# Kernel tuning notes

Hardware: AMD Instinct MI355X
Metric: run time of the kernel (lower is better)

Reference implementation:

```python
import jax, jax.numpy as jnp
import numpy as np

N_HEAD, F_IN, F_OUT = 4, 768, 64
BS, N = 4, 2048


def setup_inputs() -> dict:
    key = jax.random.key(0)
    k_h, k_w, k_src, k_dst = jax.random.split(key, 4)
    # xavier_uniform bounds
    lim_w = float(np.sqrt(6.0 / (F_IN + F_OUT)))
    lim_a = float(np.sqrt(6.0 / (F_OUT + 1)))
    return {
        "h": jax.random.normal(k_h, (BS, N, F_IN), dtype=jnp.float32),
        "w": jax.random.uniform(k_w, (N_HEAD, F_IN, F_OUT), jnp.float32, -lim_w, lim_w),
        "a_src": jax.random.uniform(k_src, (N_HEAD, F_OUT, 1), jnp.float32, -lim_a, lim_a),
        "a_dst": jax.random.uniform(k_dst, (N_HEAD, F_OUT, 1), jnp.float32, -lim_a, lim_a),
        "bias": jnp.zeros((F_OUT,), dtype=jnp.float32),
    }


def reference(h, w, a_src, a_dst, bias):
    # h: [b, n, f_in]; w: [h, f_in, f_out]
    h_prime = jnp.einsum("bnf,hfo->bhno", h, w)          # [b, h, n, f_out]
    t = jnp.tanh(h_prime)
    attn_src = jnp.einsum("bhno,ho->bhn", t, a_src[..., 0])  # [b, h, n]
    attn_dst = jnp.einsum("bhno,ho->bhn", t, a_dst[..., 0])  # [b, h, n]
    # broadcast add: attn[b,h,i,j] = src[b,h,i] + dst[b,h,j]
    attn = attn_src[..., :, None] + attn_dst[..., None, :]   # [b, h, n, n]
    attn = jnp.where(attn >= 0, attn, 0.2 * attn)            # leaky_relu(0.2)
    attn = jax.nn.softmax(attn, axis=-1)
    out = jnp.einsum("bhij,bhjo->bhio", attn, h_prime)       # [b, h, n, f_out]
    return out + bias
```

## Files before the change

kernel.cpp:

```cpp
#include <hip/hip_runtime.h>
#include <hip/hip_bf16.h>

#define NHEAD 4
#define FIN   768
#define FOUT  64
#define BSZ   4
#define NSEQ  2048
#define BH    (BSZ*NHEAD)
#define LOG2E 1.44269504088896f

typedef __attribute__((ext_vector_type(8)))  short bf16x8;
typedef __attribute__((ext_vector_type(16))) float f32x16;
typedef __attribute__((ext_vector_type(8)))  unsigned short u16x8;
typedef __attribute__((ext_vector_type(4)))  unsigned short u16x4;
typedef __attribute__((ext_vector_type(4)))  unsigned u32x4;

__device__ __forceinline__ unsigned short f2bf(float f){
  unsigned b = __float_as_uint(f);
  return (unsigned short)((b + 0x7fffu + ((b >> 16) & 1u)) >> 16);
}
__device__ __forceinline__ float fexp2(float x){
#if __has_builtin(__builtin_amdgcn_exp2f)
  return __builtin_amdgcn_exp2f(x);
#else
  return exp2f(x);
#endif
}
__device__ __forceinline__ unsigned pkbf(float lo, float hi){
#if __has_builtin(__builtin_amdgcn_cvt_pk_bf16_f32)
  typedef __attribute__((ext_vector_type(2))) __bf16 bf2;
  union { bf2 v; unsigned u; } cv;
  cv.v = __builtin_amdgcn_cvt_pk_bf16_f32(lo, hi);
  return cv.u;
#else
  return (unsigned)f2bf(lo) | ((unsigned)f2bf(hi) << 16);
#endif
}
__device__ __forceinline__ float fast_tanh(float v){
  const float e = fexp2(v * (2.0f*LOG2E));
#if __has_builtin(__builtin_amdgcn_rcpf)
  return 1.0f - 2.0f*__builtin_amdgcn_rcpf(e + 1.0f);
#else
  return 1.0f - 2.0f/(e + 1.0f);
#endif
}

__global__ __launch_bounds__(512, 4) void k_hprime(
    const float* __restrict__ h, const float* __restrict__ w,
    const float* __restrict__ a_src, const float* __restrict__ a_dst,
    unsigned short* __restrict__ hpz2, float* __restrict__ srcv,
    float* __restrict__ dstv)
{
  __shared__ __align__(16) char smem[65536];
  float* psumS = (float*)(smem + 16384);
  float* psumD = (float*)(smem + 16896);
  char*  Tt    = smem + 32768;

  const int tid  = threadIdx.x;
  const int bid  = blockIdx.x;
  const int bh1  = (bid & 7) | (((bid >> 3) & 1) << 3);
  const int head = bh1 & 3;
  const int jbase = (bid >> 4) << 6;
  const int i0a   = (bh1 >> 2)*NSEQ + jbase;
  const int wave = tid >> 6, lane = tid & 63;
  const int wm = wave & 1, wn = (wave >> 1) & 1, kw = wave >> 2;
  const int l32 = lane & 31, h32 = lane >> 5;

  f32x16 acc = {0,0,0,0,0,0,0,0,0,0,0,0,0,0,0,0};

  const int sr = tid >> 3, sc = tid & 7;
  const float* hA = h + (size_t)(i0a + sr)*FIN + sc*8;
  const int aslot = (sc ^ (sr & 7)) << 4;

  const int ob = tid & 63, cc = tid >> 6;
  const float* wsrc = w + (size_t)head*FIN*FOUT + ob;
  const int bslot0 = ((cc & 7) ^ (ob & 7)) << 4;

  float4 ra0 = *(const float4*)(hA);
  float4 ra1 = *(const float4*)(hA + 4);
  float4 ra2 = *(const float4*)(hA + 64);
  float4 ra3 = *(const float4*)(hA + 68);
  float rb[16];
  #pragma unroll
  for (int j = 0; j < 8; ++j){
    rb[j]     = wsrc[(size_t)(cc*8 + j)*FOUT];
    rb[8 + j] = wsrc[(size_t)(64 + cc*8 + j)*FOUT];
  }

  for (int it = 0; it < 6; ++it){
    char* Ab = smem +         (it & 1)*16384;
    char* Bb = smem + 32768 + (it & 1)*16384;
    u32x4 pk0, pk1;
    pk0[0] = pkbf(ra0.x, ra0.y); pk0[1] = pkbf(ra0.z, ra0.w);
    pk0[2] = pkbf(ra1.x, ra1.y); pk0[3] = pkbf(ra1.z, ra1.w);
    pk1[0] = pkbf(ra2.x, ra2.y); pk1[1] = pkbf(ra2.z, ra2.w);
    pk1[2] = pkbf(ra3.x, ra3.y); pk1[3] = pkbf(ra3.z, ra3.w);
    u32x4 qb0, qb1;
    qb0[0] = pkbf(rb[0],  rb[1]);  qb0[1] = pkbf(rb[2],  rb[3]);
    qb0[2] = pkbf(rb[4],  rb[5]);  qb0[3] = pkbf(rb[6],  rb[7]);
    qb1[0] = pkbf(rb[8],  rb[9]);  qb1[1] = pkbf(rb[10], rb[11]);
    qb1[2] = pkbf(rb[12], rb[13]); qb1[3] = pkbf(rb[14], rb[15]);
    if (it < 5){
      const float* an = hA + (it+1)*128;
      ra0 = *(const float4*)(an);      ra1 = *(const float4*)(an + 4);
      ra2 = *(const float4*)(an + 64); ra3 = *(const float4*)(an + 68);
      const float* wn_ = wsrc + (size_t)(it+1)*128*FOUT;
      #pragma unroll
      for (int j = 0; j < 8; ++j){
        rb[j]     = wn_[(size_t)(cc*8 + j)*FOUT];
        rb[8 + j] = wn_[(size_t)(64 + cc*8 + j)*FOUT];
      }
    }
    *(u32x4*)(Ab + sr*256 + aslot)        = pk0;
    *(u32x4*)(Ab + sr*256 + 128 + aslot)  = pk1;
    *(u32x4*)(Bb + ob*256 +       bslot0) = qb0;
    *(u32x4*)(Bb + ob*256 + 128 + bslot0) = qb1;
    asm volatile("s_waitcnt lgkmcnt(0)" ::: "memory");
    __builtin_amdgcn_s_barrier();
    __builtin_amdgcn_sched_barrier(0);
    #pragma unroll
    for (int s = 0; s < 4; ++s){
      const int slot = (((s*2 + h32) ^ (l32 & 7)) << 4);
      bf16x8 av = *(const bf16x8*)(Ab + (wm*32 + l32)*256 + kw*128 + slot);
      bf16x8 bv = *(const bf16x8*)(Bb + (wn*32 + l32)*256 + kw*128 + slot);
      acc = __builtin_amdgcn_mfma_f32_32x32x16_bf16(av, bv, acc, 0, 0, 0);
    }
  }

  if (kw == 1) *(f32x16*)(smem + (size_t)((wave & 3)*64 + lane)*64) = acc;
  __syncthreads();
  if (kw == 0){
    acc += *(const f32x16*)(smem + (size_t)((wave & 3)*64 + lane)*64);
    const float as = a_src[head*64 + wn*32 + l32];
    const float ad = a_dst[head*64 + wn*32 + l32];
    #pragma unroll
    for (int rb2 = 0; rb2 < 4; ++rb2){
      const int jb = wm*32 + rb2*8 + h32*4;
      u16x4 c4;
      #pragma unroll
      for (int q = 0; q < 4; ++q){
        const float v = acc[rb2*4 + q];
        c4[q] = f2bf(v);
        const float t = fast_tanh(v);
        float ps = t*as, pd = t*ad;
        ps += __shfl_xor(ps, 1);  ps += __shfl_xor(ps, 2);  ps += __shfl_xor(ps, 4);
        ps += __shfl_xor(ps, 8);  ps += __shfl_xor(ps, 16);
        pd += __shfl_xor(pd, 1);  pd += __shfl_xor(pd, 2);  pd += __shfl_xor(pd, 4);
        pd += __shfl_xor(pd, 8);  pd += __shfl_xor(pd, 16);
        if (l32 == 0){
          psumS[(jb + q)*2 + wn] = ps;
          psumD[(jb + q)*2 + wn] = pd;
        }
      }
      const int orow = wn*32 + l32;
      const int slot = ((jb >> 3) & 7) ^ (orow & 7);
      *(u16x4*)(Tt + orow*128 + slot*16 + (jb & 7)*2) = c4;
    }
  }
  __syncthreads();

  {
    const int o = tid & 63, c = tid >> 6;
    u16x8 val = *(const u16x8*)(Tt + o*128 + ((c ^ (o & 7)) << 4));
    *(u16x8*)((char*)hpz2 + ((size_t)(bh1*256 + (jbase >> 3) + c)*64 + o)*16) = val;
  }
  if (tid < 64){
    srcv[(size_t)bh1*NSEQ + jbase + tid] = (psumS[tid*2] + psumS[tid*2 + 1]) * LOG2E;
    dstv[(size_t)bh1*NSEQ + jbase + tid] = (psumD[tid*2] + psumD[tid*2 + 1]) * LOG2E;
  }
}

__global__ __launch_bounds__(512, 4) void k_attn(
    const unsigned short* __restrict__ hpz2, const float* __restrict__ srcv,
    const float* __restrict__ dstv, const float* __restrict__ bias,
    float* __restrict__ out)
{
  __shared__ __align__(16) char smem[33792];
  float* Lbuf = (float*)(smem + 32768);

  const int tid = threadIdx.x;
  const int bid = blockIdx.x;
  const int bh  = (bid & 7) | (((bid >> 3) & 1) << 3);
  const int i0  = (bid >> 4) << 6;
  const int wave = tid >> 6, lane = tid & 63;
  const int wm = wave & 1, jw = wave >> 1;
  const int l32 = lane & 31, h32 = lane >> 5;

  const float s2 = srcv[(size_t)bh*NSEQ + i0 + wm*32 + l32];
  const float u_ = s2;
  const float v_ = 0.2f*s2;

  const u16x8* gp = (const u16x8*)((const char*)hpz2 + (size_t)bh*256*64*16);
  const u16x8* tp = gp + ((jw*4 + h32)*64 + l32);
  const float* dS = dstv + (size_t)bh*NSEQ + (jw*4 + h32)*8;

  f32x16 accO0 = {0,0,0,0,0,0,0,0,0,0,0,0,0,0,0,0};
  f32x16 accO1 = {0,0,0,0,0,0,0,0,0,0,0,0,0,0,0,0};
  float lpart = 0.f;

  u16x8 c0 = tp[0], c1 = tp[32], c2 = tp[128], c3 = tp[160];
  float4 d0 = *(const float4*)(dS);
  float4 d1 = *(const float4*)(dS + 4);
  float4 d2 = *(const float4*)(dS + 16);
  float4 d3 = *(const float4*)(dS + 20);

  for (int w = 0; w < 16; ++w){
    u16x8 n0, n1, n2, n3;
    float4 g0, g1, g2, g3;
    if (w < 15){
      const u16x8* np = tp + 1024;
      n0 = np[0]; n1 = np[32]; n2 = np[128]; n3 = np[160];
      const float* dN = dS + 128;
      g0 = *(const float4*)(dN);
      g1 = *(const float4*)(dN + 4);
      g2 = *(const float4*)(dN + 16);
      g3 = *(const float4*)(dN + 20);
    }
    {
      float e0 = fexp2(fmaxf(u_ + d0.x, fmaf(0.2f, d0.x, v_)));
      float e1 = fexp2(fmaxf(u_ + d0.y, fmaf(0.2f, d0.y, v_)));
      float e2 = fexp2(fmaxf(u_ + d0.z, fmaf(0.2f, d0.z, v_)));
      float e3 = fexp2(fmaxf(u_ + d0.w, fmaf(0.2f, d0.w, v_)));
      float e4 = fexp2(fmaxf(u_ + d1.x, fmaf(0.2f, d1.x, v_)));
      float e5 = fexp2(fmaxf(u_ + d1.y, fmaf(0.2f, d1.y, v_)));
      float e6 = fexp2(fmaxf(u_ + d1.z, fmaf(0.2f, d1.z, v_)));
      float e7 = fexp2(fmaxf(u_ + d1.w, fmaf(0.2f, d1.w, v_)));
      lpart += ((e0+e1)+(e2+e3)) + ((e4+e5)+(e6+e7));
      u32x4 pk;
      pk[0] = pkbf(e0, e1); pk[1] = pkbf(e2, e3);
      pk[2] = pkbf(e4, e5); pk[3] = pkbf(e6, e7);
      const bf16x8 pA = __builtin_bit_cast(bf16x8, pk);
      accO0 = __builtin_amdgcn_mfma_f32_32x32x16_bf16(pA, c0, accO0, 0, 0, 0);
      accO1 = __builtin_amdgcn_mfma_f32_32x32x16_bf16(pA, c1, accO1, 0, 0, 0);
    }
    {
      float e0 = fexp2(fmaxf(u_ + d2.x, fmaf(0.2f, d2.x, v_)));
      float e1 = fexp2(fmaxf(u_ + d2.y, fmaf(0.2f, d2.y, v_)));
      float e2 = fexp2(fmaxf(u_ + d2.z, fmaf(0.2f, d2.z, v_)));
      float e3 = fexp2(fmaxf(u_ + d2.w, fmaf(0.2f, d2.w, v_)));
      float e4 = fexp2(fmaxf(u_ + d3.x, fmaf(0.2f, d3.x, v_)));
      float e5 = fexp2(fmaxf(u_ + d3.y, fmaf(0.2f, d3.y, v_)));
      float e6 = fexp2(fmaxf(u_ + d3.z, fmaf(0.2f, d3.z, v_)));
      float e7 = fexp2(fmaxf(u_ + d3.w, fmaf(0.2f, d3.w, v_)));
      lpart += ((e0+e1)+(e2+e3)) + ((e4+e5)+(e6+e7));
      u32x4 pk;
      pk[0] = pkbf(e0, e1); pk[1] = pkbf(e2, e3);
      pk[2] = pkbf(e4, e5); pk[3] = pkbf(e6, e7);
      const bf16x8 pA = __builtin_bit_cast(bf16x8, pk);
      accO0 = __builtin_amdgcn_mfma_f32_32x32x16_bf16(pA, c2, accO0, 0, 0, 0);
      accO1 = __builtin_amdgcn_mfma_f32_32x32x16_bf16(pA, c3, accO1, 0, 0, 0);
    }
    tp += 1024; dS += 128;
    c0 = n0; c1 = n1; c2 = n2; c3 = n3;
    d0 = g0; d1 = g1; d2 = g2; d3 = g3;
  }

  lpart += __shfl_xor(lpart, 32);
  if (lane < 32) Lbuf[(wm*4 + jw)*32 + l32] = lpart;

  const float4 bia = *(const float4*)(bias + (tid & 15)*4);
  #pragma unroll
  for (int ph = 0; ph < 2; ++ph){
    __syncthreads();
    if (wm == ph){
      float* ob = (float*)smem;
      #pragma unroll
      for (int reg = 0; reg < 16; ++reg){
        const int m = (reg & 3) + 8*(reg >> 2) + 4*h32;
        ob[(jw*32 + m)*64 +      l32] = accO0[reg];
        ob[(jw*32 + m)*64 + 32 + l32] = accO1[reg];
      }
    }
    __syncthreads();
    {
      const int i = tid >> 4, o4 = (tid & 15)*4;
      const float* ob = (const float*)smem;
      float4 v0 = *(const float4*)(ob + (0*32 + i)*64 + o4);
      float4 v1 = *(const float4*)(ob + (1*32 + i)*64 + o4);
      float4 v2 = *(const float4*)(ob + (2*32 + i)*64 + o4);
      float4 v3 = *(const float4*)(ob + (3*32 + i)*64 + o4);
      const float l = Lbuf[(ph*4+0)*32 + i] + Lbuf[(ph*4+1)*32 + i]
                    + Lbuf[(ph*4+2)*32 + i] + Lbuf[(ph*4+3)*32 + i];
      const float r = 1.f / l;
      float4 res;
      res.x = (v0.x + v1.x + v2.x + v3.x)*r + bia.x;
      res.y = (v0.y + v1.y + v2.y + v3.y)*r + bia.y;
      res.z = (v0.z + v1.z + v2.z + v3.z)*r + bia.z;
      res.w = (v0.w + v1.w + v2.w + v3.w)*r + bia.w;
      *(float4*)(out + ((size_t)bh*NSEQ + i0 + ph*32 + i)*64 + o4) = res;
    }
  }
}

extern "C" void kernel_launch(void* const* d_in, const int* in_sizes, int n_in,
                              void* d_out, int out_size, void* d_ws, size_t ws_size,
                              hipStream_t stream)
{
  const float* h     = (const float*)d_in[0];
  const float* w     = (const float*)d_in[1];
  const float* a_src = (const float*)d_in[2];
  const float* a_dst = (const float*)d_in[3];
  const float* bias  = (const float*)d_in[4];
  float* out = (float*)d_out;

  char* ws = (char*)d_ws;
  unsigned short* hpz2 = (unsigned short*)ws;
  float* srcv = (float*)(ws + (4u<<20));
  float* dstv = (float*)(ws + (4u<<20) + (128u<<10));

  k_hprime<<<512, 512, 0, stream>>>(h, w, a_src, a_dst, hpz2, srcv, dstv);
  k_attn<<<512, 512, 0, stream>>>(hpz2, srcv, dstv, bias, out);
}
```

Baseline: 116.6 us.

## Process two query-row tiles per attention block to reuse loaded value tiles

```diff
diff --git a/kernel.cpp b/kernel.cpp
--- a/kernel.cpp
+++ b/kernel.cpp
@@ -170,33 +170,37 @@
   }
 }
 
-__global__ __launch_bounds__(512, 4) void k_attn(
+__global__ __launch_bounds__(512, 2) void k_attn(
     const unsigned short* __restrict__ hpz2, const float* __restrict__ srcv,
     const float* __restrict__ dstv, const float* __restrict__ bias,
     float* __restrict__ out)
 {
-  __shared__ __align__(16) char smem[33792];
-  float* Lbuf = (float*)(smem + 32768);
+  __shared__ __align__(16) char smem[34816];
+  float* LbufA = (float*)(smem + 32768);
+  float* LbufB = (float*)(smem + 33792);
 
   const int tid = threadIdx.x;
   const int bid = blockIdx.x;
   const int bh  = (bid & 7) | (((bid >> 3) & 1) << 3);
-  const int i0  = (bid >> 4) << 6;
+  const int i0  = (bid >> 4) << 7;
   const int wave = tid >> 6, lane = tid & 63;
   const int wm = wave & 1, jw = wave >> 1;
   const int l32 = lane & 31, h32 = lane >> 5;
 
-  const float s2 = srcv[(size_t)bh*NSEQ + i0 + wm*32 + l32];
-  const float u_ = s2;
-  const float v_ = 0.2f*s2;
+  const float sA = srcv[(size_t)bh*NSEQ + i0      + wm*32 + l32];
+  const float sB = srcv[(size_t)bh*NSEQ + i0 + 64 + wm*32 + l32];
+  const float uA = sA, vA = 0.2f*sA;
+  const float uB = sB, vB = 0.2f*sB;
 
   const u16x8* gp = (const u16x8*)((const char*)hpz2 + (size_t)bh*256*64*16);
   const u16x8* tp = gp + ((jw*4 + h32)*64 + l32);
   const float* dS = dstv + (size_t)bh*NSEQ + (jw*4 + h32)*8;
 
-  f32x16 accO0 = {0,0,0,0,0,0,0,0,0,0,0,0,0,0,0,0};
-  f32x16 accO1 = {0,0,0,0,0,0,0,0,0,0,0,0,0,0,0,0};
-  float lpart = 0.f;
+  f32x16 accA0 = {0,0,0,0,0,0,0,0,0,0,0,0,0,0,0,0};
+  f32x16 accA1 = {0,0,0,0,0,0,0,0,0,0,0,0,0,0,0,0};
+  f32x16 accB0 = {0,0,0,0,0,0,0,0,0,0,0,0,0,0,0,0};
+  f32x16 accB1 = {0,0,0,0,0,0,0,0,0,0,0,0,0,0,0,0};
+  float lpA = 0.f, lpB = 0.f;
 
   u16x8 c0 = tp[0], c1 = tp[32], c2 = tp[128], c3 = tp[160];
   float4 d0 = *(const float4*)(dS);
@@ -217,46 +221,80 @@
       g3 = *(const float4*)(dN + 20);
     }
     {
-      float e0 = fexp2(fmaxf(u_ + d0.x, fmaf(0.2f, d0.x, v_)));
-      float e1 = fexp2(fmaxf(u_ + d0.y, fmaf(0.2f, d0.y, v_)));
-      float e2 = fexp2(fmaxf(u_ + d0.z, fmaf(0.2f, d0.z, v_)));
-      float e3 = fexp2(fmaxf(u_ + d0.w, fmaf(0.2f, d0.w, v_)));
-      float e4 = fexp2(fmaxf(u_ + d1.x, fmaf(0.2f, d1.x, v_)));
-      float e5 = fexp2(fmaxf(u_ + d1.y, fmaf(0.2f, d1.y, v_)));
-      float e6 = fexp2(fmaxf(u_ + d1.z, fmaf(0.2f, d1.z, v_)));
-      float e7 = fexp2(fmaxf(u_ + d1.w, fmaf(0.2f, d1.w, v_)));
-      lpart += ((e0+e1)+(e2+e3)) + ((e4+e5)+(e6+e7));
-      u32x4 pk;
-      pk[0] = pkbf(e0, e1); pk[1] = pkbf(e2, e3);
-      pk[2] = pkbf(e4, e5); pk[3] = pkbf(e6, e7);
-      const bf16x8 pA = __builtin_bit_cast(bf16x8, pk);
-      accO0 = __builtin_amdgcn_mfma_f32_32x32x16_bf16(pA, c0, accO0, 0, 0, 0);
-      accO1 = __builtin_amdgcn_mfma_f32_32x32x16_bf16(pA, c1, accO1, 0, 0, 0);
+      float eA0 = fexp2(fmaxf(uA + d0.x, fmaf(0.2f, d0.x, vA)));
+      float eA1 = fexp2(fmaxf(uA + d0.y, fmaf(0.2f, d0.y, vA)));
+      float eA2 = fexp2(fmaxf(uA + d0.z, fmaf(0.2f, d0.z, vA)));
+      float eA3 = fexp2(fmaxf(uA + d0.w, fmaf(0.2f, d0.w, vA)));
+      float eA4 = fexp2(fmaxf(uA + d1.x, fmaf(0.2f, d1.x, vA)));
+      float eA5 = fexp2(fmaxf(uA + d1.y, fmaf(0.2f, d1.y, vA)));
+      float eA6 = fexp2(fmaxf(uA + d1.z, fmaf(0.2f, d1.z, vA)));
+      float eA7 = fexp2(fmaxf(uA + d1.w, fmaf(0.2f, d1.w, vA)));
+      lpA += ((eA0+eA1)+(eA2+eA3)) + ((eA4+eA5)+(eA6+eA7));
+      u32x4 pa;
+      pa[0] = pkbf(eA0, eA1); pa[1] = pkbf(eA2, eA3);
+      pa[2] = pkbf(eA4, eA5); pa[3] = pkbf(eA6, eA7);
+      const bf16x8 pA_ = __builtin_bit_cast(bf16x8, pa);
+      float eB0 = fexp2(fmaxf(uB + d0.x, fmaf(0.2f, d0.x, vB)));
+      float eB1 = fexp2(fmaxf(uB + d0.y, fmaf(0.2f, d0.y, vB)));
+      float eB2 = fexp2(fmaxf(uB + d0.z, fmaf(0.2f, d0.z, vB)));
+      float eB3 = fexp2(fmaxf(uB + d0.w, fmaf(0.2f, d0.w, vB)));
+      float eB4 = fexp2(fmaxf(uB + d1.x, fmaf(0.2f, d1.x, vB)));
+      float eB5 = fexp2(fmaxf(uB + d1.y, fmaf(0.2f, d1.y, vB)));
+      float eB6 = fexp2(fmaxf(uB + d1.z, fmaf(0.2f, d1.z, vB)));
+      float eB7 = fexp2(fmaxf(uB + d1.w, fmaf(0.2f, d1.w, vB)));
+      lpB += ((eB0+eB1)+(eB2+eB3)) + ((eB4+eB5)+(eB6+eB7));
+      u32x4 pb;
+      pb[0] = pkbf(eB0, eB1); pb[1] = pkbf(eB2, eB3);
+      pb[2] = pkbf(eB4, eB5); pb[3] = pkbf(eB6, eB7);
+      const bf16x8 pB_ = __builtin_bit_cast(bf16x8, pb);
+      accA0 = __builtin_amdgcn_mfma_f32_32x32x16_bf16(pA_, c0, accA0, 0, 0, 0);
+      accA1 = __builtin_amdgcn_mfma_f32_32x32x16_bf16(pA_, c1, accA1, 0, 0, 0);
+      accB0 = __builtin_amdgcn_mfma_f32_32x32x16_bf16(pB_, c0, accB0, 0, 0, 0);
+      accB1 = __builtin_amdgcn_mfma_f32_32x32x16_bf16(pB_, c1, accB1, 0, 0, 0);
     }
     {
-      float e0 = fexp2(fmaxf(u_ + d2.x, fmaf(0.2f, d2.x, v_)));
-      float e1 = fexp2(fmaxf(u_ + d2.y, fmaf(0.2f, d2.y, v_)));
-      float e2 = fexp2(fmaxf(u_ + d2.z, fmaf(0.2f, d2.z, v_)));
-      float e3 = fexp2(fmaxf(u_ + d2.w, fmaf(0.2f, d2.w, v_)));
-      float e4 = fexp2(fmaxf(u_ + d3.x, fmaf(0.2f, d3.x, v_)));
-      float e5 = fexp2(fmaxf(u_ + d3.y, fmaf(0.2f, d3.y, v_)));
-      float e6 = fexp2(fmaxf(u_ + d3.z, fmaf(0.2f, d3.z, v_)));
-      float e7 = fexp2(fmaxf(u_ + d3.w, fmaf(0.2f, d3.w, v_)));
-      lpart += ((e0+e1)+(e2+e3)) + ((e4+e5)+(e6+e7));
-      u32x4 pk;
-      pk[0] = pkbf(e0, e1); pk[1] = pkbf(e2, e3);
-      pk[2] = pkbf(e4, e5); pk[3] = pkbf(e6, e7);
-      const bf16x8 pA = __builtin_bit_cast(bf16x8, pk);
-      accO0 = __builtin_amdgcn_mfma_f32_32x32x16_bf16(pA, c2, accO0, 0, 0, 0);
-      accO1 = __builtin_amdgcn_mfma_f32_32x32x16_bf16(pA, c3, accO1, 0, 0, 0);
+      float eA0 = fexp2(fmaxf(uA + d2.x, fmaf(0.2f, d2.x, vA)));
+      float eA1 = fexp2(fmaxf(uA + d2.y, fmaf(0.2f, d2.y, vA)));
+      float eA2 = fexp2(fmaxf(uA + d2.z, fmaf(0.2f, d2.z, vA)));
+      float eA3 = fexp2(fmaxf(uA + d2.w, fmaf(0.2f, d2.w, vA)));
+      float eA4 = fexp2(fmaxf(uA + d3.x, fmaf(0.2f, d3.x, vA)));
+      float eA5 = fexp2(fmaxf(uA + d3.y, fmaf(0.2f, d3.y, vA)));
+      float eA6 = fexp2(fmaxf(uA + d3.z, fmaf(0.2f, d3.z, vA)));
+      float eA7 = fexp2(fmaxf(uA + d3.w, fmaf(0.2f, d3.w, vA)));
+      lpA += ((eA0+eA1)+(eA2+eA3)) + ((eA4+eA5)+(eA6+eA7));
+      u32x4 pa;
+      pa[0] = pkbf(eA0, eA1); pa[1] = pkbf(eA2, eA3);
+      pa[2] = pkbf(eA4, eA5); pa[3] = pkbf(eA6, eA7);
+      const bf16x8 pA_ = __builtin_bit_cast(bf16x8, pa);
+      float eB0 = fexp2(fmaxf(uB + d2.x, fmaf(0.2f, d2.x, vB)));
+      float eB1 = fexp2(fmaxf(uB + d2.y, fmaf(0.2f, d2.y, vB)));
+      float eB2 = fexp2(fmaxf(uB + d2.z, fmaf(0.2f, d2.z, vB)));
+      float eB3 = fexp2(fmaxf(uB + d2.w, fmaf(0.2f, d2.w, vB)));
+      float eB4 = fexp2(fmaxf(uB + d3.x, fmaf(0.2f, d3.x, vB)));
+      float eB5 = fexp2(fmaxf(uB + d3.y, fmaf(0.2f, d3.y, vB)));
+      float eB6 = fexp2(fmaxf(uB + d3.z, fmaf(0.2f, d3.z, vB)));
+      float eB7 = fexp2(fmaxf(uB + d3.w, fmaf(0.2f, d3.w, vB)));
+      lpB += ((eB0+eB1)+(eB2+eB3)) + ((eB4+eB5)+(eB6+eB7));
+      u32x4 pb;
+      pb[0] = pkbf(eB0, eB1); pb[1] = pkbf(eB2, eB3);
+      pb[2] = pkbf(eB4, eB5); pb[3] = pkbf(eB6, eB7);
+      const bf16x8 pB_ = __builtin_bit_cast(bf16x8, pb);
+      accA0 = __builtin_amdgcn_mfma_f32_32x32x16_bf16(pA_, c2, accA0, 0, 0, 0);
+      accA1 = __builtin_amdgcn_mfma_f32_32x32x16_bf16(pA_, c3, accA1, 0, 0, 0);
+      accB0 = __builtin_amdgcn_mfma_f32_32x32x16_bf16(pB_, c2, accB0, 0, 0, 0);
+      accB1 = __builtin_amdgcn_mfma_f32_32x32x16_bf16(pB_, c3, accB1, 0, 0, 0);
     }
     tp += 1024; dS += 128;
     c0 = n0; c1 = n1; c2 = n2; c3 = n3;
     d0 = g0; d1 = g1; d2 = g2; d3 = g3;
   }
 
-  lpart += __shfl_xor(lpart, 32);
-  if (lane < 32) Lbuf[(wm*4 + jw)*32 + l32] = lpart;
+  lpA += __shfl_xor(lpA, 32);
+  lpB += __shfl_xor(lpB, 32);
+  if (lane < 32){
+    LbufA[(wm*4 + jw)*32 + l32] = lpA;
+    LbufB[(wm*4 + jw)*32 + l32] = lpB;
+  }
 
   const float4 bia = *(const float4*)(bias + (tid & 15)*4);
   #pragma unroll
@@ -267,8 +305,8 @@
       #pragma unroll
       for (int reg = 0; reg < 16; ++reg){
         const int m = (reg & 3) + 8*(reg >> 2) + 4*h32;
-        ob[(jw*32 + m)*64 +      l32] = accO0[reg];
-        ob[(jw*32 + m)*64 + 32 + l32] = accO1[reg];
+        ob[(jw*32 + m)*64 +      l32] = accA0[reg];
+        ob[(jw*32 + m)*64 + 32 + l32] = accA1[reg];
       }
     }
     __syncthreads();
@@ -279,8 +317,8 @@
       float4 v1 = *(const float4*)(ob + (1*32 + i)*64 + o4);
       float4 v2 = *(const float4*)(ob + (2*32 + i)*64 + o4);
       float4 v3 = *(const float4*)(ob + (3*32 + i)*64 + o4);
-      const float l = Lbuf[(ph*4+0)*32 + i] + Lbuf[(ph*4+1)*32 + i]
-                    + Lbuf[(ph*4+2)*32 + i] + Lbuf[(ph*4+3)*32 + i];
+      const float l = LbufA[(ph*4+0)*32 + i] + LbufA[(ph*4+1)*32 + i]
+                    + LbufA[(ph*4+2)*32 + i] + LbufA[(ph*4+3)*32 + i];
       const float r = 1.f / l;
       float4 res;
       res.x = (v0.x + v1.x + v2.x + v3.x)*r + bia.x;
@@ -288,6 +326,37 @@
       res.z = (v0.z + v1.z + v2.z + v3.z)*r + bia.z;
       res.w = (v0.w + v1.w + v2.w + v3.w)*r + bia.w;
       *(float4*)(out + ((size_t)bh*NSEQ + i0 + ph*32 + i)*64 + o4) = res;
+    }
+  }
+  #pragma unroll
+  for (int ph = 0; ph < 2; ++ph){
+    __syncthreads();
+    if (wm == ph){
+      float* ob = (float*)smem;
+      #pragma unroll
+      for (int reg = 0; reg < 16; ++reg){
+        const int m = (reg & 3) + 8*(reg >> 2) + 4*h32;
+        ob[(jw*32 + m)*64 +      l32] = accB0[reg];
+        ob[(jw*32 + m)*64 + 32 + l32] = accB1[reg];
+      }
+    }
+    __syncthreads();
+    {
+      const int i = tid >> 4, o4 = (tid & 15)*4;
+      const float* ob = (const float*)smem;
+      float4 v0 = *(const float4*)(ob + (0*32 + i)*64 + o4);
+      float4 v1 = *(const float4*)(ob + (1*32 + i)*64 + o4);
+      float4 v2 = *(const float4*)(ob + (2*32 + i)*64 + o4);
+      float4 v3 = *(const float4*)(ob + (3*32 + i)*64 + o4);
+      const float l = LbufB[(ph*4+0)*32 + i] + LbufB[(ph*4+1)*32 + i]
+                    + LbufB[(ph*4+2)*32 + i] + LbufB[(ph*4+3)*32 + i];
+      const float r = 1.f / l;
+      float4 res;
+      res.x = (v0.x + v1.x + v2.x + v3.x)*r + bia.x;
+      res.y = (v0.y + v1.y + v2.y + v3.y)*r + bia.y;
+      res.z = (v0.z + v1.z + v2.z + v3.z)*r + bia.z;
+      res.w = (v0.w + v1.w + v2.w + v3.w)*r + bia.w;
+      *(float4*)(out + ((size_t)bh*NSEQ + i0 + 64 + ph*32 + i)*64 + o4) = res;
     }
   }
 }
@@ -309,5 +378,5 @@
   float* dstv = (float*)(ws + (4u<<20) + (128u<<10));
 
   k_hprime<<<512, 512, 0, stream>>>(h, w, a_src, a_dst, hpz2, srcv, dstv);
-  k_attn<<<512, 512, 0, stream>>>(hpz2, srcv, dstv, bias, out);
-}
+  k_attn<<<256, 512, 0, stream>>>(hpz2, srcv, dstv, bias, out);
+}
```

Result: no change. 118.7 us (+1.7%).
